# Performance work log

Measured on AMD Instinct MI355X. Metric: run time of the kernel, lower is better.

The kernel has to match this reference:

```python
import jax, jax.numpy as jnp
import numpy as np
import math

D_MODEL = 512
NUM_HEADS = 8
B, L = 2, 4096
EPS_NORM = 1e-8
PLASTICITY = 1.0


def setup_inputs() -> dict:
    key = jax.random.key(0)
    ks = jax.random.split(key, 6)
    D, H = D_MODEL, NUM_HEADS
    std = 1.0 / math.sqrt(D)
    x = jax.random.normal(ks[0], (B, L, D), dtype=jnp.float32)
    qkv_w = jax.random.normal(ks[1], (3 * D, D), dtype=jnp.float32) * std
    qkv_b = jnp.zeros((3 * D,), dtype=jnp.float32)
    out_w = jax.random.normal(ks[2], (D, D), dtype=jnp.float32) * std
    out_b = jnp.zeros((D,), dtype=jnp.float32)
    decay_w = jax.random.normal(ks[3], (H, D), dtype=jnp.float32) * 0.02
    decay_b = jnp.full((H,), 4.0, dtype=jnp.float32)
    norm_scale = jnp.ones((D,), dtype=jnp.float32)
    return {"x": x, "qkv_w": qkv_w, "qkv_b": qkv_b, "out_w": out_w,
            "out_b": out_b, "decay_w": decay_w, "decay_b": decay_b,
            "norm_scale": norm_scale}


def _hebbian_forward(x, qkv_w, qkv_b, out_w, out_b, decay_w, decay_b, norm_scale):
    Bsz, Lsz, D = x.shape
    H = NUM_HEADS
    E = D // H
    # QKV projection (torch Linear: y = x @ W.T + b)
    qkv = x @ qkv_w.T + qkv_b
    q, k, v = jnp.split(qkv, 3, axis=-1)
    q = q.reshape(Bsz, Lsz, H, E)
    k = k.reshape(Bsz, Lsz, H, E)
    v = v.reshape(Bsz, Lsz, H, E)
    # feature map: elu(x) + 1
    q = (jax.nn.elu(q) + 1.0) / math.sqrt(E)
    k = jax.nn.elu(k) + 1.0
    # input-dependent decay per head
    decay_logits = x @ decay_w.T + decay_b          # (B,L,H)
    lambdas = (0.9 + 0.1 * jax.nn.sigmoid(decay_logits)) * PLASTICITY
    log_lambdas = jnp.log(jnp.clip(lambdas, 1e-6))[..., None]   # (B,L,H,1)
    log_lambda_cum = jnp.clip(jnp.cumsum(log_lambdas, axis=1), -50.0, 50.0)
    decay_k = jnp.exp(-log_lambda_cum)
    decay_q = jnp.exp(log_lambda_cum)
    k_decayed = k * decay_k
    q_decayed = q * decay_q
    # outer-product memory state cumsum: (B,L,H,E,E)
    kv = jnp.einsum('blhe,blhf->blhef', k_decayed, v)
    memory_state = jnp.cumsum(kv, axis=1)
    k_sum_decayed = jnp.cumsum(k_decayed, axis=1)
    num = jnp.einsum('blhe,blhef->blhf', q_decayed, memory_state)
    den = jnp.einsum('blhe,blhe->blh', q_decayed, k_sum_decayed)[..., None] + 1e-6
    out = (num / den).reshape(Bsz, Lsz, D)
    out = out @ out_w.T + out_b
    # RMSNorm (dropout is identity in eval)
    rnorm = jax.lax.rsqrt(jnp.mean(out * out, axis=-1, keepdims=True) + EPS_NORM)
    return out * rnorm * norm_scale


def reference(x, qkv_w, qkv_b, out_w, out_b, decay_w, decay_b, norm_scale):
    return _hebbian_forward(x, qkv_w, qkv_b, out_w, out_b, decay_w, decay_b, norm_scale)
```

## Files before the change

### kernel.cpp

```cpp
#include <hip/hip_runtime.h>

typedef unsigned short u16;
typedef unsigned int u32;

#define B_ 2
#define L_ 4096
#define D_ 512
#define H_ 8
#define E_ 64
#define M_ (B_*L_)
#define TD (3*D_)
#define NCH (L_/64)
#define BH (B_*H_)

typedef short bf16x8 __attribute__((ext_vector_type(8)));
typedef float f32x4 __attribute__((ext_vector_type(4)));

__device__ __forceinline__ float bf2f(u16 u){ return __uint_as_float(((u32)u)<<16); }
__device__ __forceinline__ u16 f2bf(float f){
  u32 u = __float_as_uint(f);
  u32 r = u + 0x7FFFu + ((u>>16)&1u);
  return (u16)(r>>16);
}
__device__ __forceinline__ float elu1(float v){ return v>0.f ? v+1.f : __expf(v); }

__device__ __forceinline__ void async_ld16(const u16* g, u16* l){
  __builtin_amdgcn_global_load_lds(
      (const __attribute__((address_space(1))) void*)g,
      (__attribute__((address_space(3))) void*)l, 16, 0, 0);
}

__global__ __launch_bounds__(256) void decay_conv_kernel(const float* __restrict__ x,
    const float* __restrict__ dw, const float* __restrict__ db,
    const float* __restrict__ qw, const float* __restrict__ ow,
    float* __restrict__ ll, u16* __restrict__ xb,
    u16* __restrict__ qwb, u16* __restrict__ owb)
{
  int blk = blockIdx.x;
  if (blk < 2048){
    int wv = threadIdx.x>>6, lane = threadIdx.x&63;
    int m = ((blk&7)<<10) + ((blk>>3)<<2) + wv;
    float xr[8];
    #pragma unroll
    for (int i=0;i<8;i++) xr[i] = x[(size_t)m*D_ + lane + 64*i];
    #pragma unroll
    for (int i=0;i<8;i++) xb[(size_t)m*D_ + lane + 64*i] = f2bf(xr[i]);
    int b = m >> 12, l = m & (L_-1);
    float acc8[8];
    #pragma unroll
    for (int h=0; h<8; h++){
      float a = 0.f;
      #pragma unroll
      for (int i=0;i<8;i++) a += xr[i]*dw[h*D_ + lane + 64*i];
      acc8[h] = a;
    }
    float s4[4];
    #pragma unroll
    for (int i=0;i<4;i++){
      float a = acc8[2*i], bb = acc8[2*i+1];
      bool odd = lane & 1;
      float keep = odd ? bb : a;
      float send = odd ? a : bb;
      s4[i] = keep + __shfl_xor(send, 1);
    }
    float s2[2];
    #pragma unroll
    for (int j=0;j<2;j++){
      float a = s4[2*j], bb = s4[2*j+1];
      bool sel = (lane>>1) & 1;
      float keep = sel ? bb : a;
      float send = sel ? a : bb;
      s2[j] = keep + __shfl_xor(send, 2);
    }
    float r;
    {
      bool sel = (lane>>2) & 1;
      float keep = sel ? s2[1] : s2[0];
      float send = sel ? s2[0] : s2[1];
      r = keep + __shfl_xor(send, 4);
    }
    r += __shfl_xor(r, 8);
    r += __shfl_xor(r, 16);
    r += __shfl_xor(r, 32);
    if (lane < 8){
      float z = r + db[lane];
      float lam = 0.9f + 0.1f/(1.f + __expf(-z));
      ll[((b*H_+lane)*L_) + l] = __logf(lam);
    }
  } else {
    int gid = (blk-2048)*256 + threadIdx.x;
    const float* src; u16* dst; int off;
    if (gid < 196608){ src = qw; dst = qwb; off = gid; }
    else { src = ow; dst = owb; off = gid - 196608; }
    float4 v = ((const float4*)src)[off];
    ushort4 o; o.x=f2bf(v.x); o.y=f2bf(v.y); o.z=f2bf(v.z); o.w=f2bf(v.w);
    ((ushort4*)dst)[off] = o;
  }
}

__global__ __launch_bounds__(256) void scan_kernel(const float* __restrict__ ll,
    float* __restrict__ cb)
{
  int bh = blockIdx.x, t = threadIdx.x;
  int lane = t & 63, wv = t >> 6;
  const float* p = ll + (size_t)bh*L_ + t*16;
  float s[16];
  #pragma unroll
  for (int q=0;q<4;q++){
    float4 v = *(const float4*)(p + q*4);
    s[q*4+0]=v.x; s[q*4+1]=v.y; s[q*4+2]=v.z; s[q*4+3]=v.w;
  }
  #pragma unroll
  for (int i=1;i<16;i++) s[i] += s[i-1];
  float tot = s[15];
  float ws = tot;
  #pragma unroll
  for (int off=1; off<64; off<<=1){
    float tmp = __shfl_up(ws, off);
    if (lane >= off) ws += tmp;
  }
  __shared__ float wsum[4];
  if (lane == 63) wsum[wv] = ws;
  __syncthreads();
  float base = 0.f;
  #pragma unroll
  for (int w2=0; w2<3; w2++) if (w2 < wv) base += wsum[w2];
  float ex = base + ws - tot;
  float* c = cb + (size_t)bh*L_ + t*16;
  #pragma unroll
  for (int i=0;i<16;i++) c[i] = fminf(50.f, fmaxf(-50.f, ex + s[i]));
}

#define BUFU 28672
#define CTS 216

__global__ __launch_bounds__(512, 2) void gemm_qkv_fused(const u16* __restrict__ A,
    const u16* __restrict__ W, const float* __restrict__ bias,
    const float* __restrict__ cb,
    u16* __restrict__ qc, u16* __restrict__ kc, u16* __restrict__ vc)
{
  __shared__ u16 SM[57344];
  int bid0 = blockIdx.x;
  int xcd = bid0 & 7, idx = bid0 >> 3;
  int mblk = xcd*4 + (idx>>3);
  int nblk = idx & 7;
  int m0 = mblk*256, n0 = nblk*192;
  int t = threadIdx.x, wave = t>>6, lane = t&63;
  int wm = (wave>>2)*128, wn = (wave&3)*48;
  int r16 = lane&15, q8h = (lane>>4);
  f32x4 acc[8][3] = {};
  int srow = t>>3, sslot = t&7;
  auto STAGE = [&](int kt, int buf){
    u16* base = SM + buf*BUFU;
    #pragma unroll
    for (int r=0;r<4;r++){
      int row = r*64 + srow;
      const u16* src = A + (size_t)(m0+row)*512 + kt*64 + ((sslot ^ (row&7))<<3);
      async_ld16(src, base + r*4096 + t*8);
    }
    #pragma unroll
    for (int r=0;r<3;r++){
      int row = r*64 + srow;
      const u16* src = W + (size_t)(n0+row)*512 + kt*64 + ((sslot ^ (row&7))<<3);
      async_ld16(src, base + 16384 + r*4096 + t*8);
    }
  };
  STAGE(0, 0);
  for (int kt=0; kt<8; kt++){
    int buf = kt & 1;
    if (kt < 7){
      STAGE(kt+1, buf^1);
      asm volatile("s_waitcnt vmcnt(7)" ::: "memory");
    } else {
      asm volatile("s_waitcnt vmcnt(0)" ::: "memory");
    }
    __builtin_amdgcn_s_barrier();
    const u16* Ab_ = SM + buf*BUFU;
    const u16* Bb_ = SM + buf*BUFU + 16384;
    bf16x8 bf[3][2];
    #pragma unroll
    for (int n=0;n<3;n++)
      #pragma unroll
      for (int ks=0;ks<2;ks++){
        int row = wn + n*16 + r16;
        int slot = (ks*4 + q8h) ^ (row&7);
        bf[n][ks] = *(const bf16x8*)&Bb_[row*64 + slot*8];
      }
    __builtin_amdgcn_s_setprio(1);
    #pragma unroll
    for (int m=0;m<8;m++){
      int row = wm + m*16 + r16;
      int s0 = q8h ^ (row&7);
      int s1 = (4 + q8h) ^ (row&7);
      bf16x8 a0 = *(const bf16x8*)&Ab_[row*64 + s0*8];
      bf16x8 a1 = *(const bf16x8*)&Ab_[row*64 + s1*8];
      #pragma unroll
      for (int n=0;n<3;n++){
        acc[m][n] = __builtin_amdgcn_mfma_f32_16x16x32_bf16(a0, bf[n][0], acc[m][n], 0,0,0);
        acc[m][n] = __builtin_amdgcn_mfma_f32_16x16x32_bf16(a1, bf[n][1], acc[m][n], 0,0,0);
      }
    }
    __builtin_amdgcn_s_setprio(0);
    __builtin_amdgcn_s_barrier();
  }
  int g = lane>>4;
  #pragma unroll
  for (int n=0;n<3;n++){
    int col = wn + n*16 + r16;
    float bv = bias[n0 + col];
    #pragma unroll
    for (int m=0;m<8;m++){
      int rb = wm + m*16 + g*4;
      #pragma unroll
      for (int r=0;r<4;r++)
        SM[(rb+r)*CTS + col] = f2bf(acc[m][n][r] + bv);
    }
  }
  __syncthreads();
  #pragma unroll
  for (int u=0;u<12;u++){
    int idx2 = t + 512*u;
    int rloc = idx2 / 24;
    int colg = (idx2 % 24) * 8;
    int row = m0 + rloc;
    int nc = n0 + colg;
    int sec = nc >> 9;
    int nn = nc & 511;
    int h2 = nn>>6, e0 = nn&63;
    int bh2 = ((row>>12)<<3) | h2;
    int bidc = (bh2<<6) | ((row>>6)&63);
    int l6 = row & 63;
    union { uint4 v; u16 s[8]; } dat;
    dat.v = *(const uint4*)&SM[rloc*CTS + colg];
    size_t a = ((size_t)(bidc*2 + (e0>>5)))*2048 + (size_t)l6*32 + (e0&31);
    if (sec == 0){
      float eqc = __expf(cb[((size_t)bh2<<12) | (row & 4095)])*0.125f;
      #pragma unroll
      for (int jj=0;jj<8;jj++) dat.s[jj] = f2bf(elu1(bf2f(dat.s[jj]))*eqc);
      *(uint4*)(qc + a) = dat.v;
    } else if (sec == 1){
      float ekc = __expf(-cb[((size_t)bh2<<12) | (row & 4095)]);
      #pragma unroll
      for (int jj=0;jj<8;jj++) dat.s[jj] = f2bf(elu1(bf2f(dat.s[jj]))*ekc);
      *(uint4*)(kc + a) = dat.v;
    } else {
      *(uint4*)(vc + a) = dat.v;
    }
  }
}

__device__ __forceinline__ int chunk_bid_remap(int i){
  int xcd = i & 7;
  int b = xcd >> 2, chhi = xcd & 3;
  int idx = i >> 3;
  int h = idx >> 4, chlo = idx & 15;
  int ch = (chhi<<4) | chlo;
  return (((b<<3)|h)<<6) | ch;
}

__global__ __launch_bounds__(256) void chunk_sums_kernel(const u16* __restrict__ kc,
    const u16* __restrict__ vc, u16* __restrict__ Stc, float* __restrict__ ksc)
{
  int bid = chunk_bid_remap(blockIdx.x);
  __shared__ u16 Kc[4096], Vc[4096];
  __shared__ u16 Ktl[5120], Vtl[5120];
  __shared__ float ksr[256];
  int t = threadIdx.x, w = t>>6, lane = t&63;
  {
    const u16* gk = kc + (size_t)bid*4096 + w*1024 + lane*8;
    const u16* gv = vc + (size_t)bid*4096 + w*1024 + lane*8;
    async_ld16(gk,       Kc + w*1024);
    async_ld16(gk + 512, Kc + w*1024 + 512);
    async_ld16(gv,       Vc + w*1024);
    async_ld16(gv + 512, Vc + w*1024 + 512);
  }
  __syncthreads();
  int e = t & 63, jq = t >> 6;
  {
    u16 kv[16] __attribute__((aligned(16)));
    u16 vv[16] __attribute__((aligned(16)));
    float ksum = 0.f;
    #pragma unroll
    for (int jj=0;jj<16;jj++){
      int j = jq*16+jj;
      kv[jj] = Kc[(e>>5)*2048 + j*32 + (e&31)];
      ksum += bf2f(kv[jj]);
      vv[jj] = Vc[(e>>5)*2048 + j*32 + (e&31)];
    }
    int kh2 = jq>>1, jl = (jq&1)*16;
    u16* kt = &Ktl[(kh2*64 + e)*40 + jl];
    u16* vt = &Vtl[(kh2*64 + e)*40 + jl];
    *(uint4*)kt     = *(const uint4*)&kv[0];
    *(uint4*)(kt+8) = *(const uint4*)&kv[8];
    *(uint4*)vt     = *(const uint4*)&vv[0];
    *(uint4*)(vt+8) = *(const uint4*)&vv[8];
    ksr[t] = ksum;
  }
  __syncthreads();
  int r16 = lane & 15, q8 = (lane>>4)*8;
  bf16x8 av[2];
  #pragma unroll
  for (int kh=0;kh<2;kh++)
    av[kh] = *(const bf16x8*)&Vtl[(kh*64 + w*16 + r16)*40 + q8];
  f32x4 acc[4] = {};
  #pragma unroll
  for (int et=0;et<4;et++)
    #pragma unroll
    for (int kh=0;kh<2;kh++){
      bf16x8 bv = *(const bf16x8*)&Ktl[(kh*64 + et*16 + r16)*40 + q8];
      acc[et] = __builtin_amdgcn_mfma_f32_16x16x32_bf16(av[kh], bv, acc[et], 0,0,0);
    }
  #pragma unroll
  for (int et=0;et<4;et++){
    int eh = et>>1, el = (et&1)*16 + r16;
    #pragma unroll
    for (int r=0;r<4;r++){
      int f = w*16 + (lane>>4)*4 + r;
      Stc[((size_t)bid*2 + eh)*2048 + f*32 + el] = f2bf(acc[et][r]);
    }
  }
  if (t < 64) ksc[bid*64 + t] = ksr[t] + ksr[64+t] + ksr[128+t] + ksr[192+t];
}

__global__ __launch_bounds__(256) void chunk_prefix_kernel(u16* __restrict__ Stc,
    float* __restrict__ ksc)
{
  int blk = blockIdx.x, t = threadIdx.x;
  if (blk < 128){
    int gid = blk*256 + t;
    int bh = gid >> 11, e2 = gid & 2047;
    u32* p = (u32*)Stc + (size_t)bh*131072 + e2;
    float r0 = 0.f, r1 = 0.f;
    #pragma unroll 16
    for (int ch=0; ch<NCH; ch++){
      u32 v = p[ch*2048];
      float lo = bf2f((u16)(v & 0xffffu));
      float hi = bf2f((u16)(v >> 16));
      p[ch*2048] = (u32)f2bf(r0) | ((u32)f2bf(r1) << 16);
      r0 += lo; r1 += hi;
    }
  } else {
    int gid2 = (blk-128)*256 + t;
    int bh2 = gid2 >> 6, e = gid2 & 63;
    float* kp = ksc + bh2*4096 + e;
    float kr = 0.f;
    #pragma unroll 8
    for (int ch=0; ch<NCH; ch++){
      float v = kp[ch*64]; kp[ch*64] = kr; kr += v;
    }
  }
}

__global__ __launch_bounds__(256) void chunk_out_kernel(const u16* __restrict__ qc,
    const u16* __restrict__ kc, const u16* __restrict__ vc,
    const u16* __restrict__ Stc, const float* __restrict__ ksc,
    u16* __restrict__ attn)
{
  int bid = chunk_bid_remap(blockIdx.x);
  int bh = bid >> 6, ch = bid & 63;
  int b = bh >> 3, h = bh & 7;
  __shared__ u16 Kb_l[4096];
  __shared__ u16 Vc_l[4096];
  __shared__ u16 Vt[5120];
  __shared__ u16 Ab[4096];
  __shared__ float R2[320];
  int t = threadIdx.x, w = t>>6, lane = t&63;
  size_t mbase = (size_t)b*L_ + ch*64;
  {
    const u16* gk = kc  + (size_t)bid*4096 + w*1024 + lane*8;
    const u16* gv = vc  + (size_t)bid*4096 + w*1024 + lane*8;
    async_ld16(gk,       Kb_l + w*1024);
    async_ld16(gk + 512, Kb_l + w*1024 + 512);
    async_ld16(gv,       Vc_l + w*1024);
    async_ld16(gv + 512, Vc_l + w*1024 + 512);
  }
  int r16 = lane & 15, q8 = (lane>>4)*8;
  const u16* qg = qc  + (size_t)bid*4096;
  const u16* sg = Stc + (size_t)bid*4096;
  bf16x8 aq[2], sfr[2][4];
  #pragma unroll
  for (int eh=0;eh<2;eh++){
    aq[eh] = *(const bf16x8*)(qg + eh*2048 + (w*16 + r16)*32 + q8);
    #pragma unroll
    for (int ft=0;ft<4;ft++)
      sfr[eh][ft] = *(const bf16x8*)(sg + (eh*64 + ft*16 + r16)*32 + q8);
  }
  int l4 = t>>2, q4 = t&3;
  int ehd = q4>>1, el0 = (q4&1)*16;
  bf16x8 x1 = *(const bf16x8*)(qg + ehd*2048 + l4*32 + el0);
  bf16x8 x2 = *(const bf16x8*)(qg + ehd*2048 + l4*32 + el0 + 8);
  union { float4 v[4]; float f[16]; } kp;
  #pragma unroll
  for (int qq=0;qq<4;qq++)
    kp.v[qq] = *(const float4*)(ksc + bid*64 + q4*16 + qq*4);
  __syncthreads();
  {
    int e = t & 63, jq = t >> 6;
    u16 vv[16] __attribute__((aligned(16)));
    #pragma unroll
    for (int jj=0;jj<16;jj++)
      vv[jj] = Vc_l[(e>>5)*2048 + (jq*16+jj)*32 + (e&31)];
    int jh = jq>>1, jl = (jq&1)*16;
    u16* vt = &Vt[(jh*64 + e)*40 + jl];
    *(uint4*)vt     = *(const uint4*)&vv[0];
    *(uint4*)(vt+8) = *(const uint4*)&vv[8];
  }
  f32x4 accA[4] = {};
  #pragma unroll
  for (int jt=0;jt<4;jt++)
    #pragma unroll
    for (int eh=0;eh<2;eh++){
      bf16x8 bv = *(const bf16x8*)&Kb_l[(eh*64 + jt*16 + r16)*32 + q8];
      accA[jt] = __builtin_amdgcn_mfma_f32_16x16x32_bf16(aq[eh], bv, accA[jt], 0,0,0);
    }
  float dkp = 0.f;
  #pragma unroll
  for (int i=0;i<8;i++)
    dkp += bf2f((u16)x1[i])*kp.f[i] + bf2f((u16)x2[i])*kp.f[8+i];
  #pragma unroll
  for (int jt=0;jt<4;jt++)
    #pragma unroll
    for (int r=0;r<4;r++){
      int lr = w*16 + ((lane>>4)<<2) + r;
      int j  = jt*16 + r16;
      Ab[((jt>>1)*64 + lr)*32 + (jt&1)*16 + r16] = (j <= lr) ? f2bf(accA[jt][r]) : (u16)0;
    }
  __syncthreads();
  float dA = 0.f;
  {
    int jh2 = q4>>1, jl0 = (q4&1)*16;
    bf16x8 y1 = *(const bf16x8*)&Ab[(jh2*64 + l4)*32 + jl0];
    bf16x8 y2 = *(const bf16x8*)&Ab[(jh2*64 + l4)*32 + jl0 + 8];
    #pragma unroll
    for (int i=0;i<8;i++) dA += bf2f((u16)y1[i]) + bf2f((u16)y2[i]);
  }
  R2[t] = dkp + dA;
  __syncthreads();
  if (t < 64) R2[256+t] = R2[t*4] + R2[t*4+1] + R2[t*4+2] + R2[t*4+3] + 1e-6f;
  bf16x8 aA[2];
  #pragma unroll
  for (int jh=0;jh<2;jh++)
    aA[jh] = *(const bf16x8*)&Ab[(jh*64 + w*16 + r16)*32 + q8];
  f32x4 acc[4] = {};
  #pragma unroll
  for (int ft=0;ft<4;ft++){
    #pragma unroll
    for (int jh=0;jh<2;jh++){
      bf16x8 bv = *(const bf16x8*)&Vt[(jh*64 + ft*16 + r16)*40 + q8];
      acc[ft] = __builtin_amdgcn_mfma_f32_16x16x32_bf16(aA[jh], bv, acc[ft], 0,0,0);
    }
    #pragma unroll
    for (int eh=0;eh<2;eh++)
      acc[ft] = __builtin_amdgcn_mfma_f32_16x16x32_bf16(aq[eh], sfr[eh][ft], acc[ft], 0,0,0);
  }
  __syncthreads();
  float inv[4];
  #pragma unroll
  for (int r=0;r<4;r++) inv[r] = 1.f / R2[256 + w*16 + ((lane>>4)<<2) + r];
  #pragma unroll
  for (int ft=0;ft<4;ft++)
    #pragma unroll
    for (int r=0;r<4;r++){
      int lr = w*16 + ((lane>>4)<<2) + r;
      attn[(mbase + lr)*D_ + h*64 + ft*16 + r16] = f2bf(acc[ft][r]*inv[r]);
    }
}

__global__ __launch_bounds__(256) void gemm_rms_kernel(const u16* __restrict__ A,
    const u16* __restrict__ W, const float* __restrict__ bias,
    const float* __restrict__ gnorm, float* __restrict__ out)
{
  __shared__ u16 As[2][1024];
  __shared__ u16 Bs[2][16384];
  __shared__ float ssq_l[4][32];
  __shared__ float rinv_l[32];
  int m0 = blockIdx.x*32;
  int t = threadIdx.x, wave = t>>6, lane = t&63;
  int wn = wave*128;
  int r16 = lane&15, q8 = (lane>>4)*8;
  f32x4 acc[2][8] = {};
  int scol = (t&3)*8;
  const u16* gB = W + (size_t)(t>>2)*512 + scol;
  const u16* gA = A + (size_t)(m0 + (t>>2))*512 + scol;
  {
    if (wave < 2) async_ld16(gA, As[0] + wave*512);
    #pragma unroll
    for (int it=0; it<8; it++)
      async_ld16(gB + it*32768, Bs[0] + wave*512 + it*2048);
  }
  int cur = 0;
  for (int k0=0; k0<512; k0+=32){
    asm volatile("s_waitcnt vmcnt(0)" ::: "memory");
    __builtin_amdgcn_s_barrier();
    if (k0 < 480){
      if (wave < 2) async_ld16(gA + k0+32, As[cur^1] + wave*512);
      #pragma unroll
      for (int it=0; it<8; it++)
        async_ld16(gB + k0+32 + it*32768, Bs[cur^1] + wave*512 + it*2048);
    }
    bf16x8 af0 = *(const bf16x8*)&As[cur][r16*32 + q8];
    bf16x8 af1 = *(const bf16x8*)&As[cur][(16 + r16)*32 + q8];
    #pragma unroll
    for (int j=0;j<8;j++){
      bf16x8 bv = *(const bf16x8*)&Bs[cur][(wn + j*16 + r16)*32 + q8];
      acc[0][j] = __builtin_amdgcn_mfma_f32_16x16x32_bf16(af0, bv, acc[0][j], 0,0,0);
      acc[1][j] = __builtin_amdgcn_mfma_f32_16x16x32_bf16(af1, bv, acc[1][j], 0,0,0);
    }
    cur ^= 1;
  }
  int g = lane>>4;
  float bv8[8], gv8[8];
  #pragma unroll
  for (int j=0;j<8;j++){ int col = wn + j*16 + r16; bv8[j] = bias[col]; gv8[j] = gnorm[col]; }
  float ssq[2][4] = {};
  #pragma unroll
  for (int i=0;i<2;i++)
    #pragma unroll
    for (int j=0;j<8;j++)
      #pragma unroll
      for (int r=0;r<4;r++){
        float v = acc[i][j][r] + bv8[j];
        acc[i][j][r] = v;
        ssq[i][r] += v*v;
      }
  #pragma unroll
  for (int off=1; off<16; off<<=1)
    #pragma unroll
    for (int i=0;i<2;i++)
      #pragma unroll
      for (int r=0;r<4;r++)
        ssq[i][r] += __shfl_xor(ssq[i][r], off);
  if (r16 == 0){
    #pragma unroll
    for (int i=0;i<2;i++)
      #pragma unroll
      for (int r=0;r<4;r++)
        ssq_l[wave][i*16 + g*4 + r] = ssq[i][r];
  }
  __syncthreads();
  if (t < 32)
    rinv_l[t] = rsqrtf((ssq_l[0][t]+ssq_l[1][t]+ssq_l[2][t]+ssq_l[3][t])*(1.f/512.f) + 1e-8f);
  __syncthreads();
  #pragma unroll
  for (int i=0;i<2;i++)
    #pragma unroll
    for (int r=0;r<4;r++){
      int row = m0 + i*16 + g*4 + r;
      float ri = rinv_l[i*16 + g*4 + r];
      #pragma unroll
      for (int j=0;j<8;j++)
        out[(size_t)row*512 + wn + j*16 + r16] = acc[i][j][r]*ri*gv8[j];
    }
}

extern "C" void kernel_launch(void* const* d_in, const int* in_sizes, int n_in,
                              void* d_out, int out_size, void* d_ws, size_t ws_size,
                              hipStream_t stream)
{
  const float* x     = (const float*)d_in[0];
  const float* w_qkv = (const float*)d_in[1];
  const float* b_qkv = (const float*)d_in[2];
  const float* w_out = (const float*)d_in[3];
  const float* b_out = (const float*)d_in[4];
  const float* w_dec = (const float*)d_in[5];
  const float* b_dec = (const float*)d_in[6];
  const float* gnorm = (const float*)d_in[7];
  float* out = (float*)d_out;

  char* ws = (char*)d_ws;
  u16*   qc   = (u16*)(ws);
  u16*   kc   = (u16*)(ws + 8388608);
  u16*   vc   = (u16*)(ws + 16777216);
  u16*   Stc  = (u16*)(ws + 25165824);
  float* ksc  = (float*)(ws + 33554432);
  float* ll   = (float*)(ws + 33816576);
  float* cb   = (float*)(ws + 34078720);
  u16*   xb   = (u16*)(ws + 34340864);
  u16*   qwb  = (u16*)(ws + 42729472);
  u16*   owb  = (u16*)(ws + 44302336);
  u16*   attn = xb;

  decay_conv_kernel<<<dim3(3072), dim3(256), 0, stream>>>(x, w_dec, b_dec, w_qkv, w_out,
                                                          ll, xb, qwb, owb);
  scan_kernel<<<dim3(BH), dim3(256), 0, stream>>>(ll, cb);
  gemm_qkv_fused<<<dim3(256), dim3(512), 0, stream>>>(xb, qwb, b_qkv, cb, qc, kc, vc);
  chunk_sums_kernel<<<dim3(BH*NCH), dim3(256), 0, stream>>>(kc, vc, Stc, ksc);
  chunk_prefix_kernel<<<dim3(132), dim3(256), 0, stream>>>(Stc, ksc);
  chunk_out_kernel<<<dim3(BH*NCH), dim3(256), 0, stream>>>(qc, kc, vc, Stc, ksc, attn);
  gemm_rms_kernel<<<dim3(M_/32), dim3(256), 0, stream>>>(attn, owb, b_out, gnorm, out);
}
```

Baseline: 153.1 us.

## Interleave QKV GEMM prefetch with MFMA phases and vectorize decay and attn stores

The QKV GEMM main loop is split into four phases per k-tile. Each phase issues part of the next tile's async global-to-LDS loads alongside the A-fragment reads and MFMAs, using extra barriers and a full vmcnt(0) wait at the top of each tile. The decay/convert kernel switches to contiguous float4 loads and uint4 bf16 stores per lane, which also changes the column ownership used by the dot products. The attention kernel now stages its output tile through LDS and writes coalesced 16-byte rows instead of scattered 2-byte stores, at the cost of an extra syncthreads.

```diff
diff --git a/kernel.cpp b/kernel.cpp
--- a/kernel.cpp
+++ b/kernel.cpp
@@ -41,18 +41,26 @@
     int wv = threadIdx.x>>6, lane = threadIdx.x&63;
     int m = ((blk&7)<<10) + ((blk>>3)<<2) + wv;
     float xr[8];
-    #pragma unroll
-    for (int i=0;i<8;i++) xr[i] = x[(size_t)m*D_ + lane + 64*i];
-    #pragma unroll
-    for (int i=0;i<8;i++) xb[(size_t)m*D_ + lane + 64*i] = f2bf(xr[i]);
+    {
+      float4 v0 = *(const float4*)&x[(size_t)m*D_ + lane*8];
+      float4 v1 = *(const float4*)&x[(size_t)m*D_ + lane*8 + 4];
+      xr[0]=v0.x; xr[1]=v0.y; xr[2]=v0.z; xr[3]=v0.w;
+      xr[4]=v1.x; xr[5]=v1.y; xr[6]=v1.z; xr[7]=v1.w;
+    }
+    {
+      union { uint4 v; u16 s[8]; } o;
+      #pragma unroll
+      for (int i=0;i<8;i++) o.s[i] = f2bf(xr[i]);
+      *(uint4*)&xb[(size_t)m*D_ + lane*8] = o.v;
+    }
     int b = m >> 12, l = m & (L_-1);
     float acc8[8];
     #pragma unroll
     for (int h=0; h<8; h++){
-      float a = 0.f;
-      #pragma unroll
-      for (int i=0;i<8;i++) a += xr[i]*dw[h*D_ + lane + 64*i];
-      acc8[h] = a;
+      const float4* dp = (const float4*)&dw[h*D_ + lane*8];
+      float4 w0 = dp[0], w1 = dp[1];
+      acc8[h] = xr[0]*w0.x + xr[1]*w0.y + xr[2]*w0.z + xr[3]*w0.w
+              + xr[4]*w1.x + xr[5]*w1.y + xr[6]*w1.z + xr[7]*w1.w;
     }
     float s4[4];
     #pragma unroll
@@ -150,59 +158,65 @@
   int r16 = lane&15, q8h = (lane>>4);
   f32x4 acc[8][3] = {};
   int srow = t>>3, sslot = t&7;
-  auto STAGE = [&](int kt, int buf){
+  auto STAGE1 = [&](int kt, int buf, int r){
     u16* base = SM + buf*BUFU;
-    #pragma unroll
-    for (int r=0;r<4;r++){
+    if (r < 4){
       int row = r*64 + srow;
       const u16* src = A + (size_t)(m0+row)*512 + kt*64 + ((sslot ^ (row&7))<<3);
       async_ld16(src, base + r*4096 + t*8);
-    }
-    #pragma unroll
-    for (int r=0;r<3;r++){
-      int row = r*64 + srow;
+    } else {
+      int rb = r-4;
+      int row = rb*64 + srow;
       const u16* src = W + (size_t)(n0+row)*512 + kt*64 + ((sslot ^ (row&7))<<3);
-      async_ld16(src, base + 16384 + r*4096 + t*8);
+      async_ld16(src, base + 16384 + rb*4096 + t*8);
     }
   };
-  STAGE(0, 0);
+  #pragma unroll
+  for (int r=0;r<7;r++) STAGE1(0, 0, r);
   for (int kt=0; kt<8; kt++){
     int buf = kt & 1;
-    if (kt < 7){
-      STAGE(kt+1, buf^1);
-      asm volatile("s_waitcnt vmcnt(7)" ::: "memory");
-    } else {
-      asm volatile("s_waitcnt vmcnt(0)" ::: "memory");
-    }
-    __builtin_amdgcn_s_barrier();
     const u16* Ab_ = SM + buf*BUFU;
     const u16* Bb_ = SM + buf*BUFU + 16384;
+    asm volatile("s_waitcnt vmcnt(0)" ::: "memory");
+    __builtin_amdgcn_s_barrier();
     bf16x8 bf[3][2];
     #pragma unroll
-    for (int n=0;n<3;n++)
-      #pragma unroll
-      for (int ks=0;ks<2;ks++){
-        int row = wn + n*16 + r16;
-        int slot = (ks*4 + q8h) ^ (row&7);
-        bf[n][ks] = *(const bf16x8*)&Bb_[row*64 + slot*8];
+    for (int p=0;p<4;p++){
+      int rowA0 = wm + (2*p)*16 + r16;
+      int rowA1 = wm + (2*p+1)*16 + r16;
+      bf16x8 a00 = *(const bf16x8*)&Ab_[rowA0*64 + ((q8h     ^ (rowA0&7))<<3)];
+      bf16x8 a01 = *(const bf16x8*)&Ab_[rowA0*64 + (((4+q8h) ^ (rowA0&7))<<3)];
+      bf16x8 a10 = *(const bf16x8*)&Ab_[rowA1*64 + ((q8h     ^ (rowA1&7))<<3)];
+      bf16x8 a11 = *(const bf16x8*)&Ab_[rowA1*64 + (((4+q8h) ^ (rowA1&7))<<3)];
+      if (p == 0){
+        #pragma unroll
+        for (int n=0;n<3;n++)
+          #pragma unroll
+          for (int ks=0;ks<2;ks++){
+            int row = wn + n*16 + r16;
+            bf[n][ks] = *(const bf16x8*)&Bb_[row*64 + (((ks*4+q8h) ^ (row&7))<<3)];
+          }
       }
-    __builtin_amdgcn_s_setprio(1);
-    #pragma unroll
-    for (int m=0;m<8;m++){
-      int row = wm + m*16 + r16;
-      int s0 = q8h ^ (row&7);
-      int s1 = (4 + q8h) ^ (row&7);
-      bf16x8 a0 = *(const bf16x8*)&Ab_[row*64 + s0*8];
-      bf16x8 a1 = *(const bf16x8*)&Ab_[row*64 + s1*8];
+      if (kt < 7){
+        if (p < 3){ STAGE1(kt+1, buf^1, 2*p); STAGE1(kt+1, buf^1, 2*p+1); }
+        else      { STAGE1(kt+1, buf^1, 6); }
+      }
+      __builtin_amdgcn_s_barrier();
+      asm volatile("s_waitcnt lgkmcnt(0)" ::: "memory");
+      __builtin_amdgcn_sched_barrier(0);
+      __builtin_amdgcn_s_setprio(1);
       #pragma unroll
       for (int n=0;n<3;n++){
-        acc[m][n] = __builtin_amdgcn_mfma_f32_16x16x32_bf16(a0, bf[n][0], acc[m][n], 0,0,0);
-        acc[m][n] = __builtin_amdgcn_mfma_f32_16x16x32_bf16(a1, bf[n][1], acc[m][n], 0,0,0);
+        acc[2*p][n]   = __builtin_amdgcn_mfma_f32_16x16x32_bf16(a00, bf[n][0], acc[2*p][n], 0,0,0);
+        acc[2*p][n]   = __builtin_amdgcn_mfma_f32_16x16x32_bf16(a01, bf[n][1], acc[2*p][n], 0,0,0);
+        acc[2*p+1][n] = __builtin_amdgcn_mfma_f32_16x16x32_bf16(a10, bf[n][0], acc[2*p+1][n], 0,0,0);
+        acc[2*p+1][n] = __builtin_amdgcn_mfma_f32_16x16x32_bf16(a11, bf[n][1], acc[2*p+1][n], 0,0,0);
       }
-    }
-    __builtin_amdgcn_s_setprio(0);
-    __builtin_amdgcn_s_barrier();
-  }
+      __builtin_amdgcn_s_setprio(0);
+      __builtin_amdgcn_s_barrier();
+    }
+  }
+  __syncthreads();
   int g = lane>>4;
   #pragma unroll
   for (int n=0;n<3;n++){
@@ -462,8 +476,14 @@
     #pragma unroll
     for (int r=0;r<4;r++){
       int lr = w*16 + ((lane>>4)<<2) + r;
-      attn[(mbase + lr)*D_ + h*64 + ft*16 + r16] = f2bf(acc[ft][r]*inv[r]);
-    }
+      Ab[lr*64 + ft*16 + r16] = f2bf(acc[ft][r]*inv[r]);
+    }
+  __syncthreads();
+  {
+    int row = t>>2, cg = (t&3)*16;
+    *(uint4*)&attn[(mbase + row)*D_ + h*64 + cg]     = *(const uint4*)&Ab[row*64 + cg];
+    *(uint4*)&attn[(mbase + row)*D_ + h*64 + cg + 8] = *(const uint4*)&Ab[row*64 + cg + 8];
+  }
 }
 
 __global__ __launch_bounds__(256) void gemm_rms_kernel(const u16* __restrict__ A,
```

Measured after the change: 153.5 us. About the same (+0.3%).
